# Performance work log

Measured on AMD Instinct MI355X. Metric: run time of the kernel, lower is better.

Reference implementation:

```python
import jax, jax.numpy as jnp
import numpy as np

N, H, G = 500_000, 128, 50_000


def setup_inputs() -> dict:
    key = jax.random.key(0)
    k1, k2, k3, k4, k5, k6, k7 = jax.random.split(key, 7)
    x_src = jax.random.normal(k1, (N, H), dtype=jnp.float32)
    imputed_embs = jax.random.normal(k2, (G, H), dtype=jnp.float32)
    src_ids = jnp.sort(jax.random.randint(k3, (N,), 0, G, dtype=jnp.int32))
    s = 1.0 / np.sqrt(2 * H)
    W1 = jax.random.uniform(k4, (H, 2 * H), jnp.float32, -s, s)  # cat_linear1
    b1 = jax.random.uniform(k5, (H,), jnp.float32, -s, s)
    W2 = jax.random.uniform(k6, (H, 2 * H), jnp.float32, -s, s)  # cat_linear2
    b2 = jax.random.uniform(k7, (H,), jnp.float32, -s, s)
    return {"x_src": x_src, "imputed_embs": imputed_embs, "W1": W1, "b1": b1,
            "W2": W2, "b2": b2, "src_ids": src_ids}


def reference(x_src, imputed_embs, W1, b1, W2, b2, src_ids):
    n, h = x_src.shape
    g = imputed_embs.shape[0]
    # group index per row: boundaries where adjacent sorted src_ids differ
    boundary = jnp.concatenate([jnp.zeros((1,), jnp.int32),
                                (src_ids[1:] != src_ids[:-1]).astype(jnp.int32)])
    gid = jnp.cumsum(boundary)  # [N] group id (0..num_groups-1)
    # segment mean of x_src per group (parallel replacement of the python loop)
    seg_sum = jax.ops.segment_sum(x_src, gid, num_segments=g)
    counts = jax.ops.segment_sum(jnp.ones((n,), x_src.dtype), gid, num_segments=g)
    seg_mean = seg_sum / jnp.maximum(counts, 1.0)[:, None]
    # original loop never writes the mean for the LAST group (or unused rows):
    written = (jnp.arange(g) < gid[-1])[:, None]
    imp_second = jnp.where(written, seg_mean, imputed_embs)
    # x_out rows: [x_src_i, imputed_embs[group(i)]]
    x_cat = jnp.concatenate([x_src, imputed_embs[gid]], axis=1)      # [N, 2H]
    imp_cat = jnp.concatenate([imputed_embs, imp_second], axis=1)    # [G, 2H]
    x_out = x_cat @ W1.T + b1
    imputed_out = imp_cat @ W2.T + b2
    return (x_out, imputed_out)
```

## Files before the change

### kernel.cpp

```cpp
#include <hip/hip_runtime.h>

typedef __attribute__((ext_vector_type(8))) short short8;
typedef __attribute__((ext_vector_type(4))) float f32x4;

static __device__ __forceinline__ unsigned short f2bf(float f) {
    union { float f; unsigned int u; } v; v.f = f;
    unsigned int r = v.u + 0x7fffu + ((v.u >> 16) & 1u);
    return (unsigned short)(r >> 16);
}

static __device__ __forceinline__ short8 pack8(float4 a, float4 b) {
    short8 r;
    r[0] = (short)f2bf(a.x); r[1] = (short)f2bf(a.y);
    r[2] = (short)f2bf(a.z); r[3] = (short)f2bf(a.w);
    r[4] = (short)f2bf(b.x); r[5] = (short)f2bf(b.y);
    r[6] = (short)f2bf(b.z); r[7] = (short)f2bf(b.w);
    return r;
}

static __device__ __forceinline__ void dma16(const void* g, void* l) {
    __builtin_amdgcn_global_load_lds(
        (const __attribute__((address_space(1))) unsigned int*)g,
        (__attribute__((address_space(3))) unsigned int*)l, 16, 0, 0);
}

static __device__ __forceinline__ float4 lds_rd16(const float* buf, int boff, int sw) {
    return *(const float4*)((const char*)buf + (boff ^ sw));
}

__global__ void k_zero(uint4* p, int n16) {
    int i = blockIdx.x * blockDim.x + threadIdx.x;
    if (i < n16) p[i] = uint4{0u, 0u, 0u, 0u};
}

__global__ void k_convw(const float* __restrict__ W1, const float* __restrict__ W2,
                        unsigned short* W1af, unsigned short* W1bf,
                        unsigned short* W2af, unsigned short* W2bf) {
    int T = blockIdx.x * 256 + threadIdx.x;
    int mat = T >> 11;
    int rem = T & 2047;
    int f = rem >> 6, lane = rem & 63;
    int wc = f >> 4, t = (f >> 2) & 3, kk = f & 3;
    int p = lane & 15, q = lane >> 4;
    int row = wc * 64 + t * 16 + p;
    int col = (mat & 1) * 128 + kk * 32 + q * 8;
    const float* src = (mat < 2 ? W1 : W2) + row * 256 + col;
    unsigned short* dst = (mat == 0 ? W1af : mat == 1 ? W1bf : mat == 2 ? W2af : W2bf);
    short8 v;
#pragma unroll
    for (int j = 0; j < 8; ++j) v[j] = (short)f2bf(src[j]);
    *(short8*)&dst[(size_t)f * 512 + lane * 8] = v;
}

__global__ void k_mark(const int* __restrict__ ids, int* __restrict__ cum, int n) {
    int i = blockIdx.x * blockDim.x + threadIdx.x;
    if (i < n) cum[ids[i]] = 1;
}

__global__ __launch_bounds__(256) void k_scan1(int* __restrict__ cum, int* __restrict__ bsum, int G) {
    __shared__ int ws[4];
    int tid = threadIdx.x;
    int base = blockIdx.x * 1024 + tid * 4;
    int a0 = 0, a1 = 0, a2 = 0, a3 = 0;
    if (base + 0 < G) a0 = cum[base + 0];
    if (base + 1 < G) a1 = cum[base + 1];
    if (base + 2 < G) a2 = cum[base + 2];
    if (base + 3 < G) a3 = cum[base + 3];
    int s = a0 + a1 + a2 + a3;
    int lane = tid & 63;
    int v = s;
#pragma unroll
    for (int off = 1; off < 64; off <<= 1) {
        int u = __shfl_up(v, off, 64);
        if (lane >= off) v += u;
    }
    if (lane == 63) ws[tid >> 6] = v;
    __syncthreads();
    int wof = 0;
    for (int w = 0; w < (tid >> 6); ++w) wof += ws[w];
    int excl = wof + v - s;
    int r0 = excl + a0, r1 = r0 + a1, r2 = r1 + a2, r3 = r2 + a3;
    if (base + 0 < G) cum[base + 0] = r0;
    if (base + 1 < G) cum[base + 1] = r1;
    if (base + 2 < G) cum[base + 2] = r2;
    if (base + 3 < G) cum[base + 3] = r3;
    if (tid == 255) bsum[blockIdx.x] = excl + s;
}

__global__ void k_scan2(int* __restrict__ bsum, int nb) {
    int t = threadIdx.x;
    int v = (t < nb) ? bsum[t] : 0;
#pragma unroll
    for (int off = 1; off < 64; off <<= 1) {
        int u = __shfl_up(v, off, 64);
        if (t >= off) v += u;
    }
    if (t < nb) bsum[t] = v;
}

__global__ void k_gid(const int* __restrict__ ids, const int* __restrict__ cum,
                      const int* __restrict__ bsum, int* __restrict__ gid,
                      int* __restrict__ gstart, int* __restrict__ ngr, int n) {
    int i = blockIdx.x * blockDim.x + threadIdx.x;
    if (i >= n) return;
    int v = ids[i];
    int blk = v >> 10;
    int g = cum[v] + (blk ? bsum[blk - 1] : 0) - 1;
    gid[i] = g;
    if (i == 0 || ids[i - 1] != v) gstart[g] = i;
    if (i == n - 1) { gstart[g + 1] = n; *ngr = g + 1; }
}

__global__ __launch_bounds__(256, 2) void k_egemm(
    const float* __restrict__ emb, const unsigned short* __restrict__ Wf,
    const float* __restrict__ b1, float* __restrict__ E1, int G) {
    __shared__ __align__(16) float ebuf[16384];
    int tid = threadIdx.x, lane = tid & 63, wid = tid >> 6;
    int p = lane & 15, q = lane >> 4;
    int wr = wid >> 1, wc = wid & 1;
    int row0 = blockIdx.x * 128;

    short8 bfr[4][4];
#pragma unroll
    for (int t = 0; t < 4; ++t)
#pragma unroll
        for (int kk = 0; kk < 4; ++kk)
            bfr[t][kk] = *(const short8*)&Wf[(size_t)((wc * 4 + t) * 4 + kk) * 512 + lane * 8];
    float b1v[4];
#pragma unroll
    for (int t = 0; t < 4; ++t) b1v[t] = b1[wc * 64 + t * 16 + p];

    long long maxb = (long long)G * 512 - 16;
#pragma unroll
    for (int k = 0; k < 16; ++k) {
        int doff = k * 4096 + tid * 16;
        int r = doff >> 9;
        long long s = (long long)(row0 + r) * 512 + (long long)((doff & 511) ^ ((r & 7) << 4));
        s = s < maxb ? s : maxb;
        dma16((const char*)emb + s, (char*)ebuf + doff);
    }
    asm volatile("s_waitcnt vmcnt(0)" ::: "memory");
    __builtin_amdgcn_s_barrier();
    __builtin_amdgcn_sched_barrier(0);

    int sw = (p & 7) << 4;
#pragma unroll
    for (int tt = 0; tt < 4; ++tt) {
        int lr = wr * 64 + tt * 16 + p;
        short8 afr[4];
#pragma unroll
        for (int kk = 0; kk < 4; ++kk) {
            int boff = lr * 512 + kk * 128 + q * 32;
            float4 v0 = lds_rd16(ebuf, boff, sw);
            float4 v1 = lds_rd16(ebuf, boff + 16, sw);
            afr[kk] = pack8(v0, v1);
        }
        f32x4 acc[4];
#pragma unroll
        for (int t = 0; t < 4; ++t) acc[t] = f32x4{0.f, 0.f, 0.f, 0.f};
#pragma unroll
        for (int t = 0; t < 4; ++t)
#pragma unroll
            for (int kk = 0; kk < 4; ++kk)
                acc[t] = __builtin_amdgcn_mfma_f32_16x16x32_bf16(afr[kk], bfr[t][kk], acc[t], 0, 0, 0);
#pragma unroll
        for (int t = 0; t < 4; ++t) {
            int colb = wc * 64 + t * 16 + p;
#pragma unroll
            for (int rg = 0; rg < 4; ++rg) {
                int rr = row0 + wr * 64 + tt * 16 + q * 4 + rg;
                if (rr < G) E1[(size_t)rr * 128 + colb] = acc[t][rg] + b1v[t];
            }
        }
    }
}

__global__ __launch_bounds__(256, 4) void k_xgemm(
    const float* __restrict__ x, const unsigned short* __restrict__ Wf,
    const int* __restrict__ gid, const float* __restrict__ E1,
    const int* __restrict__ ngr,
    float* __restrict__ out, unsigned short* __restrict__ imps,
    float* __restrict__ segsum, int N, int nwg) {
    __shared__ __align__(16) float xbuf[8192];
    __shared__ int gids[64];
    int tid = threadIdx.x, lane = tid & 63, wid = tid >> 6;
    int p = lane & 15, q = lane >> 4;
    int wr = wid >> 1, wc = wid & 1;
    int orig = blockIdx.x;
    int qq = nwg >> 3, rr8 = nwg & 7;
    int xcd = orig & 7, idx = orig >> 3;
    int bid = (xcd < rr8 ? xcd * (qq + 1) : rr8 * (qq + 1) + (xcd - rr8) * qq) + idx;
    int row0 = bid * 64;

    short8 bfr[4][4];
#pragma unroll
    for (int t = 0; t < 4; ++t)
#pragma unroll
        for (int kk = 0; kk < 4; ++kk)
            bfr[t][kk] = *(const short8*)&Wf[(size_t)((wc * 4 + t) * 4 + kk) * 512 + lane * 8];

    int gt[2];
#pragma unroll
    for (int tt = 0; tt < 2; ++tt)
        gt[tt] = gid[min(row0 + wr * 32 + tt * 16 + p, N - 1)];

    int c = tid & 127, h = tid >> 7;
    int lo = row0 + h * 32;
    int hi = min(lo + 32, N);
    int gbefore = -1, gafter = -1;
    if (lo > 0 && lo < N) gbefore = gid[lo - 1];
    if (hi < N) gafter = gid[hi];

    long long maxb = (long long)N * 512 - 16;
#pragma unroll
    for (int k = 0; k < 8; ++k) {
        int doff = k * 4096 + tid * 16;
        int r = doff >> 9;
        long long s = (long long)(row0 + r) * 512 + (long long)((doff & 511) ^ ((r & 7) << 4));
        s = s < maxb ? s : maxb;
        dma16((const char*)x + s, (char*)xbuf + doff);
    }
    if (wc == 0) {
#pragma unroll
        for (int tt = 0; tt < 2; ++tt)
            gids[wr * 32 + tt * 16 + p] = gt[tt];
    }
    asm volatile("s_waitcnt vmcnt(0) lgkmcnt(0)" ::: "memory");
    __builtin_amdgcn_s_barrier();
    __builtin_amdgcn_sched_barrier(0);

    int sw = (p & 7) << 4;
#pragma unroll
    for (int tt = 0; tt < 2; ++tt) {
        int lr = wr * 32 + tt * 16 + p;
        short8 afr[4];
#pragma unroll
        for (int kk = 0; kk < 4; ++kk) {
            int boff = lr * 512 + kk * 128 + q * 32;
            float4 v0 = lds_rd16(xbuf, boff, sw);
            float4 v1 = lds_rd16(xbuf, boff + 16, sw);
            afr[kk] = pack8(v0, v1);
        }
        int g4[4];
#pragma unroll
        for (int rg = 0; rg < 4; ++rg) g4[rg] = __shfl(gt[tt], q * 4 + rg);
        float ev[4][4];
#pragma unroll
        for (int t = 0; t < 4; ++t) {
            int colb = wc * 64 + t * 16 + p;
#pragma unroll
            for (int rg = 0; rg < 4; ++rg)
                ev[t][rg] = E1[(size_t)g4[rg] * 128 + colb];
        }
        f32x4 acc[4];
#pragma unroll
        for (int t = 0; t < 4; ++t) acc[t] = f32x4{0.f, 0.f, 0.f, 0.f};
#pragma unroll
        for (int t = 0; t < 4; ++t)
#pragma unroll
            for (int kk = 0; kk < 4; ++kk)
                acc[t] = __builtin_amdgcn_mfma_f32_16x16x32_bf16(afr[kk], bfr[t][kk], acc[t], 0, 0, 0);
#pragma unroll
        for (int t = 0; t < 4; ++t) {
            int colb = wc * 64 + t * 16 + p;
#pragma unroll
            for (int rg = 0; rg < 4; ++rg) {
                int rr = row0 + wr * 32 + tt * 16 + q * 4 + rg;
                if (rr < N) out[(size_t)rr * 128 + colb] = acc[t][rg] + ev[t][rg];
            }
        }
    }

    if (lo < N) {
        int nwin = hi - lo;
        int gbase = h * 32;
        int ng = *ngr;
        int gcur = gids[gbase];
        bool open_left = (gcur == gbefore);
        int rs = lo;
        float s = 0.f;
        for (int bb = 0; bb < nwin; bb += 8) {
            float v[8];
            int gn[8];
#pragma unroll
            for (int j = 0; j < 8; ++j) {
                int rr = bb + j; rr = rr < nwin - 1 ? rr : nwin - 1;
                int lrr = gbase + rr;
                v[j] = *(const float*)((const char*)xbuf + lrr * 512 + ((c * 4) ^ ((lrr & 7) << 4)));
                int rn = bb + j + 1; rn = rn < nwin - 1 ? rn : nwin - 1;
                gn[j] = gids[gbase + rn];
            }
#pragma unroll
            for (int j = 0; j < 8; ++j) {
                int r = bb + j;
                if (r < nwin) {
                    s += v[j];
                    bool at_end = (r + 1 >= nwin);
                    int gnext = at_end ? gafter : gn[j];
                    if (at_end || gnext != gcur) {
                        bool open_right = at_end && (gafter == gcur);
                        if (!open_left && !open_right) {
                            if (gcur < ng - 1)
                                imps[(size_t)gcur * 128 + c] = f2bf(s / (float)(lo + r + 1 - rs));
                        } else {
                            atomicAdd(&segsum[(size_t)gcur * 128 + c], s);
                        }
                        s = 0.f; rs = lo + r + 1; gcur = gnext; open_left = false;
                    }
                }
            }
        }
    }
}

__global__ __launch_bounds__(256) void k_fix(
    const float* __restrict__ segsum, const float* __restrict__ emb,
    const int* __restrict__ gstart, const int* __restrict__ ngr,
    unsigned short* __restrict__ imps, int G) {
    int g = blockIdx.x * 4 + (threadIdx.x >> 6);
    int lane = threadIdx.x & 63;
    if (g >= G) return;
    int ng = *ngr;
    float2 m;
    if (g < ng - 1) {
        int a = gstart[g], b = gstart[g + 1];
        if ((a >> 5) == ((b - 1) >> 5)) return;
        float inv = 1.0f / (float)(b - a);
        float2 s = *(const float2*)&segsum[(size_t)g * 128 + lane * 2];
        m.x = s.x * inv; m.y = s.y * inv;
    } else {
        m = *(const float2*)&emb[(size_t)g * 128 + lane * 2];
    }
    unsigned int pk = (unsigned int)f2bf(m.x) | ((unsigned int)f2bf(m.y) << 16);
    ((unsigned int*)imps)[(size_t)g * 64 + lane] = pk;
}

__global__ __launch_bounds__(256, 2) void k_igemm(
    const float* __restrict__ emb, const unsigned short* __restrict__ imps,
    const unsigned short* __restrict__ Waf, const unsigned short* __restrict__ Wbf,
    const float* __restrict__ b2, float* __restrict__ out2, int G) {
    __shared__ __align__(16) float ebuf[8192];
    __shared__ __align__(16) unsigned short ibuf[8192];
    int tid = threadIdx.x, lane = tid & 63, wid = tid >> 6;
    int p = lane & 15, q = lane >> 4;
    int wr = wid >> 1, wc = wid & 1;
    int row0 = blockIdx.x * 64;

    short8 bfrA[4][4], bfrB[4][4];
#pragma unroll
    for (int t = 0; t < 4; ++t)
#pragma unroll
        for (int kk = 0; kk < 4; ++kk) {
            bfrA[t][kk] = *(const short8*)&Waf[(size_t)((wc * 4 + t) * 4 + kk) * 512 + lane * 8];
            bfrB[t][kk] = *(const short8*)&Wbf[(size_t)((wc * 4 + t) * 4 + kk) * 512 + lane * 8];
        }
    float b2v[4];
#pragma unroll
    for (int t = 0; t < 4; ++t) b2v[t] = b2[wc * 64 + t * 16 + p];

    long long maxe = (long long)G * 512 - 16;
    long long maxi = (long long)G * 256 - 16;
#pragma unroll
    for (int k = 0; k < 8; ++k) {
        int doff = k * 4096 + tid * 16;
        int r = doff >> 9;
        long long s = (long long)(row0 + r) * 512 + (long long)((doff & 511) ^ ((r & 7) << 4));
        s = s < maxe ? s : maxe;
        dma16((const char*)emb + s, (char*)ebuf + doff);
    }
#pragma unroll
    for (int k = 0; k < 4; ++k) {
        int doff = k * 4096 + tid * 16;
        int r = doff >> 8;
        long long s = (long long)(row0 + r) * 256 + (long long)((doff & 255) ^ ((r & 7) << 4));
        s = s < maxi ? s : maxi;
        dma16((const char*)imps + s, (char*)ibuf + doff);
    }
    asm volatile("s_waitcnt vmcnt(0)" ::: "memory");
    __builtin_amdgcn_s_barrier();
    __builtin_amdgcn_sched_barrier(0);

    int sw = (p & 7) << 4;
#pragma unroll
    for (int tt = 0; tt < 2; ++tt) {
        int lr = wr * 32 + tt * 16 + p;
        short8 ae[4], ia[4];
#pragma unroll
        for (int kk = 0; kk < 4; ++kk) {
            int boff = lr * 512 + kk * 128 + q * 32;
            float4 v0 = lds_rd16(ebuf, boff, sw);
            float4 v1 = lds_rd16(ebuf, boff + 16, sw);
            ae[kk] = pack8(v0, v1);
            int boff2 = lr * 256 + ((kk * 64 + q * 16) ^ sw);
            ia[kk] = *(const short8*)((const char*)ibuf + boff2);
        }
        f32x4 acc[4];
#pragma unroll
        for (int t = 0; t < 4; ++t) acc[t] = f32x4{0.f, 0.f, 0.f, 0.f};
#pragma unroll
        for (int kk = 0; kk < 4; ++kk)
#pragma unroll
            for (int t = 0; t < 4; ++t) {
                acc[t] = __builtin_amdgcn_mfma_f32_16x16x32_bf16(ae[kk], bfrA[t][kk], acc[t], 0, 0, 0);
                acc[t] = __builtin_amdgcn_mfma_f32_16x16x32_bf16(ia[kk], bfrB[t][kk], acc[t], 0, 0, 0);
            }
#pragma unroll
        for (int t = 0; t < 4; ++t) {
            int colb = wc * 64 + t * 16 + p;
#pragma unroll
            for (int rg = 0; rg < 4; ++rg) {
                int rr = row0 + wr * 32 + tt * 16 + q * 4 + rg;
                if (rr < G) out2[(size_t)rr * 128 + colb] = acc[t][rg] + b2v[t];
            }
        }
    }
}

extern "C" void kernel_launch(void* const* d_in, const int* in_sizes, int n_in,
                              void* d_out, int out_size, void* d_ws, size_t ws_size,
                              hipStream_t stream) {
    const float* x   = (const float*)d_in[0];
    const float* emb = (const float*)d_in[1];
    const float* W1  = (const float*)d_in[2];
    const float* b1  = (const float*)d_in[3];
    const float* W2  = (const float*)d_in[4];
    const float* b2  = (const float*)d_in[5];
    const int*   ids = (const int*)d_in[6];
    const int H = 128;
    const int N = in_sizes[6];
    const int G = in_sizes[1] / H;

    float* out  = (float*)d_out;
    float* out2 = out + (size_t)N * H;
    float* E1   = out2;

    char* ws = (char*)d_ws;
    size_t off = 0;
    float* segsum = (float*)(ws + off); off += (size_t)G * H * 4;
    int*   cum    = (int*)(ws + off);   off += (size_t)G * 4;
    size_t zbytes = off;
    off = (off + 255) & ~(size_t)255;
    int* bsum   = (int*)(ws + off); off += 64 * 4;          off = (off + 255) & ~(size_t)255;
    int* gid    = (int*)(ws + off); off += (size_t)N * 4;   off = (off + 255) & ~(size_t)255;
    int* gstart = (int*)(ws + off); off += (size_t)(G + 1) * 4; off = (off + 255) & ~(size_t)255;
    int* ngr    = (int*)(ws + off); off += 256;
    unsigned short* W1af = (unsigned short*)(ws + off); off += (size_t)H * H * 2;
    unsigned short* W1bf = (unsigned short*)(ws + off); off += (size_t)H * H * 2;
    unsigned short* W2af = (unsigned short*)(ws + off); off += (size_t)H * H * 2;
    unsigned short* W2bf = (unsigned short*)(ws + off); off += (size_t)H * H * 2;
    unsigned short* imps = (unsigned short*)(ws + off); off += (size_t)G * H * 2;

    int n16 = (int)((zbytes + 15) / 16);
    int nb = (G + 1023) >> 10;
    int nwgX = (N + 63) >> 6;
    int nwgE = (G + 127) >> 7;
    int nwgI = (G + 63) >> 6;
    k_zero<<<(n16 + 255) / 256, 256, 0, stream>>>((uint4*)ws, n16);
    k_convw<<<32, 256, 0, stream>>>(W1, W2, W1af, W1bf, W2af, W2bf);
    k_mark<<<(N + 255) / 256, 256, 0, stream>>>(ids, cum, N);
    k_scan1<<<nb, 256, 0, stream>>>(cum, bsum, G);
    k_scan2<<<1, 64, 0, stream>>>(bsum, nb);
    k_gid<<<(N + 255) / 256, 256, 0, stream>>>(ids, cum, bsum, gid, gstart, ngr, N);
    k_egemm<<<nwgE, 256, 0, stream>>>(emb, W1bf, b1, E1, G);
    k_xgemm<<<nwgX, 256, 0, stream>>>(x, W1af, gid, E1, ngr, out, imps, segsum, N, nwgX);
    k_fix<<<(G + 3) / 4, 256, 0, stream>>>(segsum, emb, gstart, ngr, imps, G);
    k_igemm<<<nwgI, 256, 0, stream>>>(emb, imps, W2af, W2bf, b2, out2, G);
}
```

Before: 197.6 us.

## Store E1 in bf16 workspace, shrink egemm tiles, split xgemm load wait

The per-group embedding projection E1 is now written as bf16 into a separate workspace buffer instead of fp32 into the output, which halves the bytes the x GEMM has to gather per row. The egemm kernel moves to 64-row tiles with a smaller LDS footprint and a higher occupancy bound. In xgemm the row mapping is reordered so the first 16-row slab of each wave arrives in the first half of the DMA loads. The kernel now waits only on those loads, computes the first slab, then waits for the rest before the second slab, overlapping load latency with MFMA work. The cost is extra bf16 rounding on the E1 term and a second barrier.

```diff
diff --git a/kernel.cpp b/kernel.cpp
--- a/kernel.cpp
+++ b/kernel.cpp
@@ -7,6 +7,10 @@
     union { float f; unsigned int u; } v; v.f = f;
     unsigned int r = v.u + 0x7fffu + ((v.u >> 16) & 1u);
     return (unsigned short)(r >> 16);
+}
+
+static __device__ __forceinline__ float bf2f(unsigned short b) {
+    union { unsigned int u; float f; } v; v.u = (unsigned int)b << 16; return v.f;
 }
 
 static __device__ __forceinline__ short8 pack8(float4 a, float4 b) {
@@ -111,14 +115,14 @@
     if (i == n - 1) { gstart[g + 1] = n; *ngr = g + 1; }
 }
 
-__global__ __launch_bounds__(256, 2) void k_egemm(
+__global__ __launch_bounds__(256, 4) void k_egemm(
     const float* __restrict__ emb, const unsigned short* __restrict__ Wf,
-    const float* __restrict__ b1, float* __restrict__ E1, int G) {
-    __shared__ __align__(16) float ebuf[16384];
+    const float* __restrict__ b1, unsigned short* __restrict__ E1b, int G) {
+    __shared__ __align__(16) float ebuf[8192];
     int tid = threadIdx.x, lane = tid & 63, wid = tid >> 6;
     int p = lane & 15, q = lane >> 4;
     int wr = wid >> 1, wc = wid & 1;
-    int row0 = blockIdx.x * 128;
+    int row0 = blockIdx.x * 64;
 
     short8 bfr[4][4];
 #pragma unroll
@@ -132,7 +136,7 @@
 
     long long maxb = (long long)G * 512 - 16;
 #pragma unroll
-    for (int k = 0; k < 16; ++k) {
+    for (int k = 0; k < 8; ++k) {
         int doff = k * 4096 + tid * 16;
         int r = doff >> 9;
         long long s = (long long)(row0 + r) * 512 + (long long)((doff & 511) ^ ((r & 7) << 4));
@@ -145,8 +149,8 @@
 
     int sw = (p & 7) << 4;
 #pragma unroll
-    for (int tt = 0; tt < 4; ++tt) {
-        int lr = wr * 64 + tt * 16 + p;
+    for (int tt = 0; tt < 2; ++tt) {
+        int lr = wr * 32 + tt * 16 + p;
         short8 afr[4];
 #pragma unroll
         for (int kk = 0; kk < 4; ++kk) {
@@ -168,8 +172,8 @@
             int colb = wc * 64 + t * 16 + p;
 #pragma unroll
             for (int rg = 0; rg < 4; ++rg) {
-                int rr = row0 + wr * 64 + tt * 16 + q * 4 + rg;
-                if (rr < G) E1[(size_t)rr * 128 + colb] = acc[t][rg] + b1v[t];
+                int rr = row0 + wr * 32 + tt * 16 + q * 4 + rg;
+                if (rr < G) E1b[(size_t)rr * 128 + colb] = f2bf(acc[t][rg] + b1v[t]);
             }
         }
     }
@@ -177,7 +181,7 @@
 
 __global__ __launch_bounds__(256, 4) void k_xgemm(
     const float* __restrict__ x, const unsigned short* __restrict__ Wf,
-    const int* __restrict__ gid, const float* __restrict__ E1,
+    const int* __restrict__ gid, const unsigned short* __restrict__ E1b,
     const int* __restrict__ ngr,
     float* __restrict__ out, unsigned short* __restrict__ imps,
     float* __restrict__ segsum, int N, int nwg) {
@@ -202,7 +206,7 @@
     int gt[2];
 #pragma unroll
     for (int tt = 0; tt < 2; ++tt)
-        gt[tt] = gid[min(row0 + wr * 32 + tt * 16 + p, N - 1)];
+        gt[tt] = gid[min(row0 + tt * 32 + wr * 16 + p, N - 1)];
 
     int c = tid & 127, h = tid >> 7;
     int lo = row0 + h * 32;
@@ -223,16 +227,16 @@
     if (wc == 0) {
 #pragma unroll
         for (int tt = 0; tt < 2; ++tt)
-            gids[wr * 32 + tt * 16 + p] = gt[tt];
-    }
-    asm volatile("s_waitcnt vmcnt(0) lgkmcnt(0)" ::: "memory");
+            gids[tt * 32 + wr * 16 + p] = gt[tt];
+    }
+    asm volatile("s_waitcnt vmcnt(4) lgkmcnt(0)" ::: "memory");
     __builtin_amdgcn_s_barrier();
     __builtin_amdgcn_sched_barrier(0);
 
     int sw = (p & 7) << 4;
 #pragma unroll
     for (int tt = 0; tt < 2; ++tt) {
-        int lr = wr * 32 + tt * 16 + p;
+        int lr = tt * 32 + wr * 16 + p;
         short8 afr[4];
 #pragma unroll
         for (int kk = 0; kk < 4; ++kk) {
@@ -250,7 +254,7 @@
             int colb = wc * 64 + t * 16 + p;
 #pragma unroll
             for (int rg = 0; rg < 4; ++rg)
-                ev[t][rg] = E1[(size_t)g4[rg] * 128 + colb];
+                ev[t][rg] = bf2f(E1b[(size_t)g4[rg] * 128 + colb]);
         }
         f32x4 acc[4];
 #pragma unroll
@@ -265,9 +269,14 @@
             int colb = wc * 64 + t * 16 + p;
 #pragma unroll
             for (int rg = 0; rg < 4; ++rg) {
-                int rr = row0 + wr * 32 + tt * 16 + q * 4 + rg;
+                int rr = row0 + tt * 32 + wr * 16 + q * 4 + rg;
                 if (rr < N) out[(size_t)rr * 128 + colb] = acc[t][rg] + ev[t][rg];
             }
+        }
+        if (tt == 0) {
+            asm volatile("s_waitcnt vmcnt(32)" ::: "memory");
+            __builtin_amdgcn_s_barrier();
+            __builtin_amdgcn_sched_barrier(0);
         }
     }
 
@@ -432,7 +441,6 @@
 
     float* out  = (float*)d_out;
     float* out2 = out + (size_t)N * H;
-    float* E1   = out2;
 
     char* ws = (char*)d_ws;
     size_t off = 0;
@@ -449,11 +457,12 @@
     unsigned short* W2af = (unsigned short*)(ws + off); off += (size_t)H * H * 2;
     unsigned short* W2bf = (unsigned short*)(ws + off); off += (size_t)H * H * 2;
     unsigned short* imps = (unsigned short*)(ws + off); off += (size_t)G * H * 2;
+    unsigned short* E1b  = (unsigned short*)(ws + off); off += (size_t)G * H * 2;
 
     int n16 = (int)((zbytes + 15) / 16);
     int nb = (G + 1023) >> 10;
     int nwgX = (N + 63) >> 6;
-    int nwgE = (G + 127) >> 7;
+    int nwgE = (G + 63) >> 6;
     int nwgI = (G + 63) >> 6;
     k_zero<<<(n16 + 255) / 256, 256, 0, stream>>>((uint4*)ws, n16);
     k_convw<<<32, 256, 0, stream>>>(W1, W2, W1af, W1bf, W2af, W2bf);
@@ -461,8 +470,8 @@
     k_scan1<<<nb, 256, 0, stream>>>(cum, bsum, G);
     k_scan2<<<1, 64, 0, stream>>>(bsum, nb);
     k_gid<<<(N + 255) / 256, 256, 0, stream>>>(ids, cum, bsum, gid, gstart, ngr, N);
-    k_egemm<<<nwgE, 256, 0, stream>>>(emb, W1bf, b1, E1, G);
-    k_xgemm<<<nwgX, 256, 0, stream>>>(x, W1af, gid, E1, ngr, out, imps, segsum, N, nwgX);
+    k_egemm<<<nwgE, 256, 0, stream>>>(emb, W1bf, b1, E1b, G);
+    k_xgemm<<<nwgX, 256, 0, stream>>>(x, W1af, gid, E1b, ngr, out, imps, segsum, N, nwgX);
     k_fix<<<(G + 3) / 4, 256, 0, stream>>>(segsum, emb, gstart, ngr, imps, G);
     k_igemm<<<nwgI, 256, 0, stream>>>(emb, imps, W2af, W2bf, b2, out2, G);
 }
```

New measurement: 226.9 us. +14.9%, slower.
